# Performance work log

Hardware: AMD Instinct MI355X
Metric: run time of the kernel (lower is better)

The kernel has to match this reference:

```python
import jax, jax.numpy as jnp
import numpy as np

H = 1024
N_HEAD = 16
HEAD = H // N_HEAD
EPS = 1e-12


def setup_inputs() -> dict:
    key = jax.random.key(0)
    ks = jax.random.split(key, 12)
    B, S = 2, 2048
    scale = 1.0 / np.sqrt(H)
    inp = {
        "pre_out": jax.random.normal(ks[0], (B, S, H), dtype=jnp.float32),
        "att_mask": jnp.ones((B, 1, 1, S), dtype=jnp.float32),
        "Wq": jax.random.normal(ks[1], (H, H), dtype=jnp.float32) * scale,
        "bq": jnp.zeros((H,), dtype=jnp.float32),
        "Wk": jax.random.normal(ks[2], (H, H), dtype=jnp.float32) * scale,
        "bk": jnp.zeros((H,), dtype=jnp.float32),
        "Wv": jax.random.normal(ks[3], (H, H), dtype=jnp.float32) * scale,
        "bv": jnp.zeros((H,), dtype=jnp.float32),
        "Wo": jax.random.normal(ks[4], (H, H), dtype=jnp.float32) * scale,
        "bo": jnp.zeros((H,), dtype=jnp.float32),
        "ln_w": jnp.ones((H,), dtype=jnp.float32),
        "ln_b": jnp.zeros((H,), dtype=jnp.float32),
    }
    return inp


def _heads(x):
    # [B,S,H] -> [B,n_head,S,head]
    B, S, _ = x.shape
    return x.reshape(B, S, N_HEAD, HEAD).transpose(0, 2, 1, 3)


def _layernorm(x, w, b):
    u = jnp.mean(x, axis=-1, keepdims=True)
    s = jnp.mean((x - u) ** 2, axis=-1, keepdims=True)
    return w * ((x - u) / jnp.sqrt(s + EPS)) + b


def reference(pre_out, att_mask, Wq, bq, Wk, bk, Wv, bv, Wo, bo, ln_w, ln_b):
    B, S, _ = pre_out.shape
    # torch Linear: y = x @ W.T + b
    Q = _heads(pre_out @ Wq.T + bq)
    K = _heads(pre_out @ Wk.T + bk)
    V = _heads(pre_out @ Wv.T + bv)
    scores = jnp.einsum('bhqd,bhkd->bhqk', Q, K) / np.sqrt(HEAD)
    scores = scores + (1.0 - att_mask) * -10000.0
    prob = jax.nn.softmax(scores, axis=-1)  # eval mode: no dropout
    att = jnp.einsum('bhqk,bhkd->bhqd', prob, V)
    att = att.transpose(0, 2, 1, 3).reshape(B, S, H)
    out = att @ Wo.T + bo
    return _layernorm(pre_out + out, ln_w, ln_b)
```

## Files before the change

### kernel.cpp

```cpp
#include <hip/hip_runtime.h>
#include <math.h>

typedef unsigned short u16;
typedef float floatx4 __attribute__((ext_vector_type(4)));
typedef __bf16 bf16x8 __attribute__((ext_vector_type(8)));
typedef u16 u16x4 __attribute__((ext_vector_type(4)));

#define BB 2
#define SS 2048
#define HH 1024
#define NHEAD 16

__device__ __forceinline__ u16 f2bf(float f) {
  union { float f; unsigned u; } a; a.f = f;
  unsigned r = a.u + 0x7fffu + ((a.u >> 16) & 1u);
  return (u16)(r >> 16);
}

__device__ __forceinline__ u16 bfbits(float f) {
  union { __bf16 h; u16 u; } c; c.h = (__bf16)f; return c.u;
}

__device__ __forceinline__ void gload16(const u16* g, u16* l) {
  __builtin_amdgcn_global_load_lds((const __attribute__((address_space(1))) void*)g,
                                   (__attribute__((address_space(3))) void*)l, 16, 0, 0);
}

__global__ __launch_bounds__(256) void cvt_all(
    const float* __restrict__ X, const float* __restrict__ Wq, const float* __restrict__ Wk,
    const float* __restrict__ Wv, const float* __restrict__ Wo, const float* __restrict__ mask,
    u16* __restrict__ Xb, u16* __restrict__ Wqb, u16* __restrict__ Wkb,
    u16* __restrict__ Wvb, u16* __restrict__ Wob, float* __restrict__ B2) {
  int i = blockIdx.x * 256 + threadIdx.x;
  if (i >= (2 << 20)) {
    int off = i - (2 << 20);
    float4 m = ((const float4*)mask)[off];
    float4 o;
    o.x = (1.0f - m.x) * (-10000.0f * 1.44269504f);
    o.y = (1.0f - m.y) * (-10000.0f * 1.44269504f);
    o.z = (1.0f - m.z) * (-10000.0f * 1.44269504f);
    o.w = (1.0f - m.w) * (-10000.0f * 1.44269504f);
    ((float4*)B2)[off] = o;
    return;
  }
  const float* src; u16* dst; int off;
  if (i < (1 << 20)) { src = X; dst = Xb; off = i; }
  else {
    int j = i - (1 << 20);
    int m = j >> 18; off = j & ((1 << 18) - 1);
    src = (m == 0) ? Wq : (m == 1) ? Wk : (m == 2) ? Wv : Wo;
    dst = (m == 0) ? Wqb : (m == 1) ? Wkb : (m == 2) ? Wvb : Wob;
  }
  float4 v = ((const float4*)src)[off];
  u16x4 p; p.x = f2bf(v.x); p.y = f2bf(v.y); p.z = f2bf(v.z); p.w = f2bf(v.w);
  ((u16x4*)dst)[off] = p;
}

__global__ __launch_bounds__(256) void qkv_gemm(
    const u16* __restrict__ X,
    const u16* __restrict__ Wq, const u16* __restrict__ Wk, const u16* __restrict__ Wv,
    const float* __restrict__ bq, const float* __restrict__ bk, const float* __restrict__ bv,
    u16* __restrict__ Qo, u16* __restrict__ Ko, u16* __restrict__ Vt) {
  __shared__ u16 As[128 * 32];
  __shared__ u16 Ws[128 * 32];

  const int tid = threadIdx.x;
  const int w = tid >> 6, lane = tid & 63, quad = lane >> 4, l15 = lane & 15;
  const int mat = blockIdx.x >> 3;
  const int col0 = (blockIdx.x & 7) * 128;
  const int row0 = blockIdx.y * 128;
  const u16* W = (mat == 0) ? Wq : (mat == 1) ? Wk : Wv;
  const float* bias = (mat == 0) ? bq : (mat == 1) ? bk : bv;

  const int c0 = tid, c1 = tid + 256;
  const int ar0 = c0 >> 2, al0 = ((c0 & 3) ^ (ar0 & 3)) * 8;
  const int ar1 = c1 >> 2, al1 = ((c1 & 3) ^ (ar1 & 3)) * 8;
  const u16* gA0 = X + (row0 + ar0) * HH + al0;
  const u16* gA1 = X + (row0 + ar1) * HH + al1;
  const u16* gW0 = W + (col0 + ar0) * HH + al0;
  const u16* gW1 = W + (col0 + ar1) * HH + al1;
  u16* lA0 = As + c0 * 8; u16* lA1 = As + c1 * 8;
  u16* lW0 = Ws + c0 * 8; u16* lW1 = Ws + c1 * 8;

  const int wm = (w >> 1) * 64, wn = (w & 1) * 64;
  const int sw = quad ^ (l15 & 3);
  const int aoff = (wm + l15) * 32 + sw * 8;
  const int boff = (wn + l15) * 32 + sw * 8;

  floatx4 acc[4][4];
#pragma unroll
  for (int i = 0; i < 4; i++)
#pragma unroll
    for (int j = 0; j < 4; j++) acc[i][j] = {0.f, 0.f, 0.f, 0.f};

  for (int k0 = 0; k0 < HH; k0 += 32) {
    __syncthreads();
    gload16(gA0 + k0, lA0);
    gload16(gA1 + k0, lA1);
    gload16(gW0 + k0, lW0);
    gload16(gW1 + k0, lW1);
    __syncthreads();
    bf16x8 af[4], bfr[4];
#pragma unroll
    for (int i = 0; i < 4; i++) af[i] = *(const bf16x8*)(As + aoff + i * 512);
#pragma unroll
    for (int j = 0; j < 4; j++) bfr[j] = *(const bf16x8*)(Ws + boff + j * 512);
#pragma unroll
    for (int i = 0; i < 4; i++)
#pragma unroll
      for (int j = 0; j < 4; j++)
        acc[i][j] = __builtin_amdgcn_mfma_f32_16x16x32_bf16(af[i], bfr[j], acc[i][j], 0, 0, 0);
  }

  const int rb = row0 + wm + quad * 4;
  if (mat < 2) {
    u16* O = (mat == 0) ? Qo : Ko;
#pragma unroll
    for (int j = 0; j < 4; j++) {
      const int col = col0 + wn + j * 16 + l15;
      const float bj = bias[col];
#pragma unroll
      for (int i = 0; i < 4; i++) {
        const int r0 = rb + i * 16;
#pragma unroll
        for (int r = 0; r < 4; r++)
          O[(r0 + r) * HH + col] = bfbits(acc[i][j][r] + bj);
      }
    }
  } else {
#pragma unroll
    for (int j = 0; j < 4; j++) {
      const int col = col0 + wn + j * 16 + l15;
      const float bj = bias[col];
      const int h = col >> 6, d = col & 63;
#pragma unroll
      for (int i = 0; i < 4; i++) {
        const int m0 = rb + i * 16;
        const int b = m0 >> 11, s = m0 & 2047;
        u16x4 pk;
#pragma unroll
        for (int r = 0; r < 4; r++) pk[r] = bfbits(acc[i][j][r] + bj);
        *(u16x4*)(Vt + (((b * NHEAD + h) * 64 + d) * SS + s)) = pk;
      }
    }
  }
}

__global__ __launch_bounds__(256) void oproj_gemm(
    const u16* __restrict__ A, const u16* __restrict__ W,
    const float* __restrict__ bias, float* __restrict__ Y) {
  __shared__ u16 As[128 * 32];
  __shared__ u16 Ws[64 * 32];

  const int tid = threadIdx.x;
  const int w = tid >> 6, lane = tid & 63, quad = lane >> 4, l15 = lane & 15;
  const int col0 = blockIdx.x * 64;
  const int row0 = blockIdx.y * 128;

  const int c0 = tid, c1 = tid + 256;
  const int ar0 = c0 >> 2, al0 = ((c0 & 3) ^ (ar0 & 3)) * 8;
  const int ar1 = c1 >> 2, al1 = ((c1 & 3) ^ (ar1 & 3)) * 8;
  const u16* gA0 = A + (row0 + ar0) * HH + al0;
  const u16* gA1 = A + (row0 + ar1) * HH + al1;
  const u16* gW0 = W + (col0 + ar0) * HH + al0;
  u16* lA0 = As + c0 * 8; u16* lA1 = As + c1 * 8;
  u16* lW0 = Ws + c0 * 8;

  const int wm = w * 32;
  const int sw = quad ^ (l15 & 3);
  const int aoff = (wm + l15) * 32 + sw * 8;
  const int boff = l15 * 32 + sw * 8;

  floatx4 acc[2][4];
#pragma unroll
  for (int i = 0; i < 2; i++)
#pragma unroll
    for (int j = 0; j < 4; j++) acc[i][j] = {0.f, 0.f, 0.f, 0.f};

  for (int k0 = 0; k0 < HH; k0 += 32) {
    __syncthreads();
    gload16(gA0 + k0, lA0);
    gload16(gA1 + k0, lA1);
    if (tid < 256) gload16(gW0 + k0, lW0);
    __syncthreads();
    bf16x8 af[2], bfr[4];
#pragma unroll
    for (int i = 0; i < 2; i++) af[i] = *(const bf16x8*)(As + aoff + i * 512);
#pragma unroll
    for (int j = 0; j < 4; j++) bfr[j] = *(const bf16x8*)(Ws + boff + j * 512);
#pragma unroll
    for (int i = 0; i < 2; i++)
#pragma unroll
      for (int j = 0; j < 4; j++)
        acc[i][j] = __builtin_amdgcn_mfma_f32_16x16x32_bf16(af[i], bfr[j], acc[i][j], 0, 0, 0);
  }

  const int rb = row0 + wm + quad * 4;
#pragma unroll
  for (int j = 0; j < 4; j++) {
    const int col = col0 + j * 16 + l15;
    const float bj = bias[col];
#pragma unroll
    for (int i = 0; i < 2; i++) {
      const int r0 = rb + i * 16;
#pragma unroll
      for (int r = 0; r < 4; r++)
        Y[(r0 + r) * HH + col] = acc[i][j][r] + bj;
    }
  }
}

#define QT 128

__global__ __launch_bounds__(256, 3) void attn_mfma(
    const u16* __restrict__ Q, const u16* __restrict__ K, const u16* __restrict__ Vt,
    const float* __restrict__ B2, u16* __restrict__ O) {
  __shared__ u16 UQ[9216];
  __shared__ u16 Ks[64 * 64];
  __shared__ u16 Vs[64 * 64];

  const int qt = blockIdx.x, bh = blockIdx.y;
  const int b = bh >> 4, h = bh & 15;
  const int tid = threadIdx.x;
  const int w = tid >> 6, lane = tid & 63, quad = lane >> 4, l15 = lane & 15;
  const int sw = l15 & 7;

  const int qbase  = (b * SS + qt * QT) * HH + h * 64;
  const int kvbase = (b * SS) * HH + h * 64;
  const int vtbase = (b * NHEAD + h) * 64 * SS;

#pragma unroll
  for (int i = 0; i < 4; i++) {
    const int c = tid + i * 256;
    const int r = c >> 3, lc = (c & 7) ^ (r & 7);
    gload16(Q + qbase + r * HH + lc * 8, UQ + c * 8);
  }
  __syncthreads();

  bf16x8 aQ[2][2];
#pragma unroll
  for (int mt = 0; mt < 2; mt++) {
    const u16* qr = UQ + (w * 32 + mt * 16 + l15) * 64;
    aQ[mt][0] = *(const bf16x8*)(qr + ((quad ^ sw) * 8));
    aQ[mt][1] = *(const bf16x8*)(qr + (((4 + quad) ^ sw) * 8));
  }

  floatx4 o[2][4];
#pragma unroll
  for (int mt = 0; mt < 2; mt++)
#pragma unroll
    for (int j = 0; j < 4; j++) o[mt][j] = {0.f, 0.f, 0.f, 0.f};
  float lp[2] = {0.f, 0.f};

  u16* Pw = UQ + w * 2304;
  const float* B2row = B2 + b * SS;

  for (int kt = 0; kt < 32; kt++) {
    __syncthreads();
#pragma unroll
    for (int i = 0; i < 2; i++) {
      const int c = tid + i * 256;
      const int r = c >> 3, lc = (c & 7) ^ (r & 7);
      gload16(K + kvbase + (kt * 64 + r) * HH + lc * 8, Ks + c * 8);
      gload16(Vt + vtbase + r * SS + kt * 64 + lc * 8, Vs + c * 8);
    }
    __syncthreads();

    floatx4 st[2][4];
#pragma unroll
    for (int kb = 0; kb < 4; kb++) {
      const u16* kr = Ks + (kb * 16 + l15) * 64;
      bf16x8 kf0 = *(const bf16x8*)(kr + ((quad ^ sw) * 8));
      bf16x8 kf1 = *(const bf16x8*)(kr + (((4 + quad) ^ sw) * 8));
#pragma unroll
      for (int mt = 0; mt < 2; mt++) {
        floatx4 z = {0.f, 0.f, 0.f, 0.f};
        z = __builtin_amdgcn_mfma_f32_16x16x32_bf16(kf0, aQ[mt][0], z, 0, 0, 0);
        st[mt][kb] = __builtin_amdgcn_mfma_f32_16x16x32_bf16(kf1, aQ[mt][1], z, 0, 0, 0);
      }
    }

#pragma unroll
    for (int kb = 0; kb < 4; kb++) {
      const floatx4 bb = *(const floatx4*)(B2row + kt * 64 + kb * 16 + quad * 4);
#pragma unroll
      for (int mt = 0; mt < 2; mt++) {
        u16x4 pk;
#pragma unroll
        for (int r = 0; r < 4; r++) {
          const float p = __builtin_amdgcn_exp2f(st[mt][kb][r] * 0.180336880f + bb[r]);
          lp[mt] += p;
          pk[r] = bfbits(p);
        }
        *(u16x4*)(Pw + (mt * 16 + l15) * 72 + kb * 16 + quad * 4) = pk;
      }
    }

    bf16x8 pa[2][2];
#pragma unroll
    for (int mt = 0; mt < 2; mt++) {
      const u16* pr = Pw + (mt * 16 + l15) * 72;
      pa[mt][0] = *(const bf16x8*)(pr + quad * 8);
      pa[mt][1] = *(const bf16x8*)(pr + 32 + quad * 8);
    }
#pragma unroll
    for (int j = 0; j < 4; j++) {
      const u16* vr = Vs + (j * 16 + l15) * 64;
      bf16x8 v0 = *(const bf16x8*)(vr + ((quad ^ sw) * 8));
      bf16x8 v1 = *(const bf16x8*)(vr + (((4 + quad) ^ sw) * 8));
#pragma unroll
      for (int mt = 0; mt < 2; mt++) {
        o[mt][j] = __builtin_amdgcn_mfma_f32_16x16x32_bf16(pa[mt][0], v0, o[mt][j], 0, 0, 0);
        o[mt][j] = __builtin_amdgcn_mfma_f32_16x16x32_bf16(pa[mt][1], v1, o[mt][j], 0, 0, 0);
      }
    }
  }

#pragma unroll
  for (int mt = 0; mt < 2; mt++) {
    float v = lp[mt];
    v += __shfl_xor(v, 16);
    v += __shfl_xor(v, 32);
    lp[mt] = v;
  }

#pragma unroll
  for (int mt = 0; mt < 2; mt++) {
    const int orow0 = b * SS + qt * QT + w * 32 + mt * 16 + quad * 4;
#pragma unroll
    for (int r = 0; r < 4; r++) {
      const float inv = 1.0f / __shfl(lp[mt], quad * 4 + r);
#pragma unroll
      for (int j = 0; j < 4; j++)
        O[(orow0 + r) * HH + h * 64 + j * 16 + l15] = bfbits(o[mt][j][r] * inv);
    }
  }
}

__device__ __forceinline__ float block_sum256(float v) {
  __shared__ float sb[4];
#pragma unroll
  for (int o = 1; o < 64; o <<= 1) v += __shfl_xor(v, o);
  if ((threadIdx.x & 63) == 0) sb[threadIdx.x >> 6] = v;
  __syncthreads();
  float r = sb[0] + sb[1] + sb[2] + sb[3];
  __syncthreads();
  return r;
}

__global__ __launch_bounds__(256) void add_layernorm(
    const float* __restrict__ x0, const float* __restrict__ y,
    const float* __restrict__ w, const float* __restrict__ b,
    float* __restrict__ out) {
  const int row = blockIdx.x;
  const int t = threadIdx.x;
  const float* xr = x0 + (size_t)row * HH;
  const float* yr = y + (size_t)row * HH;

  float v[4];
  float sum = 0.f;
#pragma unroll
  for (int i = 0; i < 4; i++) {
    int idx = t + i * 256;
    v[i] = xr[idx] + yr[idx];
    sum += v[i];
  }
  float mean = block_sum256(sum) * (1.0f / HH);

  float sq = 0.f;
#pragma unroll
  for (int i = 0; i < 4; i++) {
    float d = v[i] - mean;
    sq += d * d;
  }
  float var = block_sum256(sq) * (1.0f / HH);
  float inv = rsqrtf(var + 1e-12f);

#pragma unroll
  for (int i = 0; i < 4; i++) {
    int idx = t + i * 256;
    out[(size_t)row * HH + idx] = w[idx] * ((v[i] - mean) * inv) + b[idx];
  }
}

extern "C" void kernel_launch(void* const* d_in, const int* in_sizes, int n_in,
                              void* d_out, int out_size, void* d_ws, size_t ws_size,
                              hipStream_t stream) {
  const float* pre_out = (const float*)d_in[0];
  const float* mask    = (const float*)d_in[1];
  const float* Wq = (const float*)d_in[2];
  const float* bq = (const float*)d_in[3];
  const float* Wk = (const float*)d_in[4];
  const float* bk = (const float*)d_in[5];
  const float* Wv = (const float*)d_in[6];
  const float* bv = (const float*)d_in[7];
  const float* Wo = (const float*)d_in[8];
  const float* bo = (const float*)d_in[9];
  const float* ln_w = (const float*)d_in[10];
  const float* ln_b = (const float*)d_in[11];
  float* out = (float*)d_out;

  u16* Xb  = (u16*)d_ws;
  u16* Wqb = Xb + (4 << 20);
  u16* Wkb = Wqb + (1 << 20);
  u16* Wvb = Wkb + (1 << 20);
  u16* Wob = Wvb + (1 << 20);
  u16* Qb  = Wob + (1 << 20);
  u16* Kb  = Qb + (4 << 20);
  u16* Vtb = Kb + (4 << 20);
  u16* Ab  = Vtb + (4 << 20);
  float* Yb = (float*)(Ab + (4 << 20));
  float* B2 = Yb + (4 << 20);

  cvt_all<<<8196, 256, 0, stream>>>(pre_out, Wq, Wk, Wv, Wo, mask,
                                    Xb, Wqb, Wkb, Wvb, Wob, B2);

  qkv_gemm<<<dim3(24, 32), 256, 0, stream>>>(Xb, Wqb, Wkb, Wvb, bq, bk, bv, Qb, Kb, Vtb);

  attn_mfma<<<dim3(SS / QT, BB * NHEAD), 256, 0, stream>>>(Qb, Kb, Vtb, B2, Ab);

  oproj_gemm<<<dim3(16, 32), 256, 0, stream>>>(Ab, Wob, bo, Yb);

  add_layernorm<<<BB * SS, 256, 0, stream>>>(pre_out, Yb, ln_w, ln_b, out);
}
```

Measured before the change: 230.2 us.

## Double-buffer K/V tiles in attention with prefetch and remap block order

The attention kernel now keeps two K/V LDS buffers and issues the global-to-LDS loads for the next key tile before computing on the current one. Explicit vmcnt waits and raw barriers replace the __syncthreads pairs, and the mask bias is loaded at the top of each iteration. The block index is also remapped so that consecutive workgroups spread across heads and batches, to change L2 locality. The extra 16KB of LDS may lower occupancy from the requested 3 blocks per CU, and the hand-counted vmcnt values must match the outstanding load counts exactly.

Measured after the change: 214.9 us. -6.7%, faster.

```diff
diff --git a/kernel.cpp b/kernel.cpp
--- a/kernel.cpp
+++ b/kernel.cpp
@@ -24,6 +24,12 @@
 __device__ __forceinline__ void gload16(const u16* g, u16* l) {
   __builtin_amdgcn_global_load_lds((const __attribute__((address_space(1))) void*)g,
                                    (__attribute__((address_space(3))) void*)l, 16, 0, 0);
+}
+
+__device__ __forceinline__ void fencebar() {
+  asm volatile("" ::: "memory");
+  __builtin_amdgcn_s_barrier();
+  asm volatile("" ::: "memory");
 }
 
 __global__ __launch_bounds__(256) void cvt_all(
@@ -216,10 +222,12 @@
     const u16* __restrict__ Q, const u16* __restrict__ K, const u16* __restrict__ Vt,
     const float* __restrict__ B2, u16* __restrict__ O) {
   __shared__ u16 UQ[9216];
-  __shared__ u16 Ks[64 * 64];
-  __shared__ u16 Vs[64 * 64];
-
-  const int qt = blockIdx.x, bh = blockIdx.y;
+  __shared__ u16 Ks[2][64 * 64];
+  __shared__ u16 Vs[2][64 * 64];
+
+  const int L = blockIdx.y * 16 + blockIdx.x;
+  const int wid = (L & 7) * 64 + (L >> 3);
+  const int qt = wid & 15, bh = wid >> 4;
   const int b = bh >> 4, h = bh & 15;
   const int tid = threadIdx.x;
   const int w = tid >> 6, lane = tid & 63, quad = lane >> 4, l15 = lane & 15;
@@ -229,13 +237,25 @@
   const int kvbase = (b * SS) * HH + h * 64;
   const int vtbase = (b * NHEAD + h) * 64 * SS;
 
+  auto stage_kv = [&](u16* kd, u16* vd, int t) {
+#pragma unroll
+    for (int i = 0; i < 2; i++) {
+      const int c = tid + i * 256;
+      const int r = c >> 3, lc = (c & 7) ^ (r & 7);
+      gload16(K + kvbase + (t * 64 + r) * HH + lc * 8, kd + c * 8);
+      gload16(Vt + vtbase + r * SS + t * 64 + lc * 8, vd + c * 8);
+    }
+  };
+
 #pragma unroll
   for (int i = 0; i < 4; i++) {
     const int c = tid + i * 256;
     const int r = c >> 3, lc = (c & 7) ^ (r & 7);
     gload16(Q + qbase + r * HH + lc * 8, UQ + c * 8);
   }
-  __syncthreads();
+  stage_kv(Ks[0], Vs[0], 0);
+  asm volatile("s_waitcnt vmcnt(4)" ::: "memory");
+  fencebar();
 
   bf16x8 aQ[2][2];
 #pragma unroll
@@ -256,20 +276,28 @@
   const float* B2row = B2 + b * SS;
 
   for (int kt = 0; kt < 32; kt++) {
-    __syncthreads();
-#pragma unroll
-    for (int i = 0; i < 2; i++) {
-      const int c = tid + i * 256;
-      const int r = c >> 3, lc = (c & 7) ^ (r & 7);
-      gload16(K + kvbase + (kt * 64 + r) * HH + lc * 8, Ks + c * 8);
-      gload16(Vt + vtbase + r * SS + kt * 64 + lc * 8, Vs + c * 8);
-    }
-    __syncthreads();
+    const int cur = kt & 1;
+    const u16* Kc = Ks[cur];
+    const u16* Vc = Vs[cur];
+
+    floatx4 bb[4];
+#pragma unroll
+    for (int kb = 0; kb < 4; kb++)
+      bb[kb] = *(const floatx4*)(B2row + kt * 64 + kb * 16 + quad * 4);
+    asm volatile("" ::: "memory");
+
+    if (kt < 31) {
+      stage_kv(Ks[cur ^ 1], Vs[cur ^ 1], kt + 1);
+      asm volatile("s_waitcnt vmcnt(4) lgkmcnt(0)" ::: "memory");
+    } else {
+      asm volatile("s_waitcnt vmcnt(0) lgkmcnt(0)" ::: "memory");
+    }
+    fencebar();
 
     floatx4 st[2][4];
 #pragma unroll
     for (int kb = 0; kb < 4; kb++) {
-      const u16* kr = Ks + (kb * 16 + l15) * 64;
+      const u16* kr = Kc + (kb * 16 + l15) * 64;
       bf16x8 kf0 = *(const bf16x8*)(kr + ((quad ^ sw) * 8));
       bf16x8 kf1 = *(const bf16x8*)(kr + (((4 + quad) ^ sw) * 8));
 #pragma unroll
@@ -282,13 +310,12 @@
 
 #pragma unroll
     for (int kb = 0; kb < 4; kb++) {
-      const floatx4 bb = *(const floatx4*)(B2row + kt * 64 + kb * 16 + quad * 4);
 #pragma unroll
       for (int mt = 0; mt < 2; mt++) {
         u16x4 pk;
 #pragma unroll
         for (int r = 0; r < 4; r++) {
-          const float p = __builtin_amdgcn_exp2f(st[mt][kb][r] * 0.180336880f + bb[r]);
+          const float p = __builtin_amdgcn_exp2f(st[mt][kb][r] * 0.180336880f + bb[kb][r]);
           lp[mt] += p;
           pk[r] = bfbits(p);
         }
@@ -305,7 +332,7 @@
     }
 #pragma unroll
     for (int j = 0; j < 4; j++) {
-      const u16* vr = Vs + (j * 16 + l15) * 64;
+      const u16* vr = Vc + (j * 16 + l15) * 64;
       bf16x8 v0 = *(const bf16x8*)(vr + ((quad ^ sw) * 8));
       bf16x8 v1 = *(const bf16x8*)(vr + (((4 + quad) ^ sw) * 8));
 #pragma unroll
@@ -314,6 +341,8 @@
         o[mt][j] = __builtin_amdgcn_mfma_f32_16x16x32_bf16(pa[mt][1], v1, o[mt][j], 0, 0, 0);
       }
     }
+
+    fencebar();
   }
 
 #pragma unroll
```
